# Performance work log

Hardware: AMD Instinct MI355X
Metric: run time of the kernel (lower is better)

The kernel has to match this reference:

```python
import jax, jax.numpy as jnp
import numpy as np

MARGIN = 0.3
EPS = 1e-12


def setup_inputs() -> dict:
    key = jax.random.key(0)
    k1, k2 = jax.random.split(key)
    inputs = jax.random.normal(k1, (256, 2048), dtype=jnp.float32)
    targets = jax.random.randint(k2, (256,), 0, 32, dtype=jnp.int64)
    return {"inputs": inputs, "targets": targets}


def reference(inputs, targets):
    # Pairwise Euclidean distance matrix [n, n] via GEMM.
    sq = jnp.sum(inputs * inputs, axis=1)                      # [n]
    dist = sq[:, None] + sq[None, :] - 2.0 * (inputs @ inputs.T)
    dist = jnp.sqrt(jnp.clip(dist, EPS, None))                 # [n, n]

    same = targets[:, None] == targets[None, :]                # [n, n]
    # Triplet margin for all (anchor, positive, negative) in one broadcast.
    tri = dist[:, :, None] - dist[:, None, :] + MARGIN         # [n, n, n]
    tri = jnp.clip(tri, EPS, None)
    # Valid: same label for (a, p), different label for (a, neg).
    valid = same[:, :, None] & (~same)[:, None, :]             # [n, n, n]
    # Torch version stacks only valid triplets (dynamic shape); here we
    # return the dense [n, n, n] tensor with invalid entries zeroed.
    return jnp.where(valid, tri, 0.0)
```

## Files before the change

### kernel.cpp

```cpp
#include <hip/hip_runtime.h>
#include <hip/hip_fp16.h>

#define N 256
#define D 2048
#define MARGIN_F 0.3f
#define EPS_F 1e-12f
#define SQRT_EPS_F 1e-6f
#define KSLICES 8

typedef float v4f __attribute__((ext_vector_type(4)));
typedef short bf16x8 __attribute__((ext_vector_type(8)));

static __device__ __forceinline__ unsigned short f2bf_rne(float f) {
    union { float f; unsigned u; } v; v.f = f;
    unsigned r = v.u + 0x7fffu + ((v.u >> 16) & 1u);
    return (unsigned short)(r >> 16);
}

__global__ __launch_bounds__(256) void conv_sq_kernel(const float* __restrict__ x,
                                                      unsigned short* __restrict__ xb,
                                                      float* __restrict__ sq) {
    __shared__ float red[4];
    const int row = blockIdx.x;
    const int tid = threadIdx.x;
    const float* xr = x + (size_t)row * D + tid * 8;
    float4 v0 = *(const float4*)(xr);
    float4 v1 = *(const float4*)(xr + 4);
    float acc = v0.x * v0.x + v0.y * v0.y + v0.z * v0.z + v0.w * v0.w +
                v1.x * v1.x + v1.y * v1.y + v1.z * v1.z + v1.w * v1.w;
    union { unsigned short h[8]; uint4 u; } pk;
    pk.h[0] = f2bf_rne(v0.x); pk.h[1] = f2bf_rne(v0.y);
    pk.h[2] = f2bf_rne(v0.z); pk.h[3] = f2bf_rne(v0.w);
    pk.h[4] = f2bf_rne(v1.x); pk.h[5] = f2bf_rne(v1.y);
    pk.h[6] = f2bf_rne(v1.z); pk.h[7] = f2bf_rne(v1.w);
    *(uint4*)(xb + (size_t)row * D + tid * 8) = pk.u;
#pragma unroll
    for (int off = 32; off > 0; off >>= 1) acc += __shfl_down(acc, off, 64);
    if ((tid & 63) == 0) red[tid >> 6] = acc;
    __syncthreads();
    if (tid == 0) sq[row] = red[0] + red[1] + red[2] + red[3];
}

__global__ __launch_bounds__(256) void gram_mfma_kernel(const unsigned short* __restrict__ xb,
                                                        float* __restrict__ part) {
    const int w = threadIdx.x >> 6;
    const int l = threadIdx.x & 63;
    const int i0 = blockIdx.x * 32 + (w >> 1) * 16;
    const int j0 = blockIdx.y * 32 + (w & 1) * 16;
    const int ks = blockIdx.z;
    const int kq = (l >> 4) * 8;
    const unsigned short* pa = xb + (size_t)(i0 + (l & 15)) * D + ks * 256 + kq;
    const unsigned short* pb = xb + (size_t)(j0 + (l & 15)) * D + ks * 256 + kq;
    v4f acc = {0.f, 0.f, 0.f, 0.f};
#pragma unroll
    for (int t = 0; t < 8; ++t) {
        bf16x8 af = *(const bf16x8*)(pa + t * 32);
        bf16x8 bf = *(const bf16x8*)(pb + t * 32);
        acc = __builtin_amdgcn_mfma_f32_16x16x32_bf16(af, bf, acc, 0, 0, 0);
    }
    float* pp = part + ((size_t)(i0 + (l >> 4) * 4) * KSLICES + ks) * N + j0 + (l & 15);
#pragma unroll
    for (int r = 0; r < 4; ++r)
        pp[(size_t)r * KSLICES * N] = acc[r];
}

__global__ __launch_bounds__(256) void fused_kernel(const float* __restrict__ part,
                                                    const float* __restrict__ sq,
                                                    const int* __restrict__ targets,
                                                    float* __restrict__ out) {
    __shared__ __align__(16) float drow[N];
    __shared__ int lab[N];
    const int a = blockIdx.x;
    const int tid = threadIdx.x;
    lab[tid] = targets[tid];

    const float* pr = part + (size_t)a * (KSLICES * N);
    float dot = 0.f;
#pragma unroll
    for (int ks = 0; ks < KSLICES; ++ks)
        dot += pr[ks * N + tid];
    drow[tid] = (tid == a) ? SQRT_EPS_F
                           : sqrtf(fmaxf(sq[a] + sq[tid] - 2.f * dot, EPS_F));
    __syncthreads();

    const int la = lab[a];
    const int lane = tid & 63;
    const int pq = tid >> 6;
    const int p0 = blockIdx.y * 64 + pq * 16;

    v4f dan = *(const v4f*)(drow + lane * 4);
    v4f mb = MARGIN_F - dan;
    v4f nokv = {(lab[lane * 4 + 0] != la) ? 1.f : 0.f,
                (lab[lane * 4 + 1] != la) ? 1.f : 0.f,
                (lab[lane * 4 + 2] != la) ? 1.f : 0.f,
                (lab[lane * 4 + 3] != la) ? 1.f : 0.f};

    float* obase = out + ((size_t)a << 16) + lane * 4;
#pragma unroll 4
    for (int i = 0; i < 16; ++i) {
        int p = p0 + i;
        v4f r = {0.f, 0.f, 0.f, 0.f};
        if (lab[p] == la) {
            float dap = drow[p];
            v4f t = dap + mb;
            t.x = fmaxf(t.x, EPS_F);
            t.y = fmaxf(t.y, EPS_F);
            t.z = fmaxf(t.z, EPS_F);
            t.w = fmaxf(t.w, EPS_F);
            r = t * nokv;
        }
        *(v4f*)(obase + (size_t)p * N) = r;
    }
}

__global__ __launch_bounds__(64) void sq_kernel(const float* __restrict__ x,
                                                float* __restrict__ sq) {
    int row = blockIdx.x;
    int lane = threadIdx.x;
    const float4* xr = (const float4*)(x + (size_t)row * D);
    float acc = 0.f;
#pragma unroll
    for (int it = 0; it < 8; ++it) {
        float4 v = xr[lane + 64 * it];
        acc += v.x * v.x + v.y * v.y + v.z * v.z + v.w * v.w;
    }
#pragma unroll
    for (int off = 32; off > 0; off >>= 1) acc += __shfl_down(acc, off, 64);
    if (lane == 0) sq[row] = acc;
}

__global__ __launch_bounds__(256) void gram_valu_kernel(const float* __restrict__ x,
                                                        __half* __restrict__ part) {
    __shared__ __align__(16) float As[64 * 68];
    __shared__ __align__(16) float Bs[64 * 68];
    const int i0 = blockIdx.x * 64, j0 = blockIdx.y * 64, k0 = blockIdx.z * 64;
    const int tid = threadIdx.x;
#pragma unroll
    for (int it = 0; it < 4; ++it) {
        int f = tid + 256 * it;
        int row = f >> 4;
        int c4 = f & 15;
        int sc4 = c4 ^ ((row >> 2) & 15);
        float4 va = *(const float4*)(x + (size_t)(i0 + row) * D + k0 + c4 * 4);
        float4 vb = *(const float4*)(x + (size_t)(j0 + row) * D + k0 + c4 * 4);
        *(float4*)(As + row * 68 + sc4 * 4) = va;
        *(float4*)(Bs + row * 68 + sc4 * 4) = vb;
    }
    __syncthreads();
    const int tx = tid & 15, ty = tid >> 4;
    float acc[4][4];
#pragma unroll
    for (int r = 0; r < 4; ++r)
#pragma unroll
        for (int c = 0; c < 4; ++c) acc[r][c] = 0.f;
#pragma unroll
    for (int k4 = 0; k4 < 16; ++k4) {
        float4 a[4], b[4];
        const int ca = (k4 ^ ty) << 2, cb = (k4 ^ tx) << 2;
#pragma unroll
        for (int r = 0; r < 4; ++r) {
            a[r] = *(const float4*)(As + (ty * 4 + r) * 68 + ca);
            b[r] = *(const float4*)(Bs + (tx * 4 + r) * 68 + cb);
        }
#pragma unroll
        for (int r = 0; r < 4; ++r)
#pragma unroll
            for (int c = 0; c < 4; ++c)
                acc[r][c] += a[r].x * b[c].x + a[r].y * b[c].y +
                             a[r].z * b[c].z + a[r].w * b[c].w;
    }
    __half* pout = part + (size_t)blockIdx.z * (N * N);
#pragma unroll
    for (int r = 0; r < 4; ++r) {
        int gi = i0 + ty * 4 + r;
        union { __half2 h2[2]; uint2 u; } pk;
        pk.h2[0] = __floats2half2_rn(acc[r][0], acc[r][1]);
        pk.h2[1] = __floats2half2_rn(acc[r][2], acc[r][3]);
        *(uint2*)(pout + (size_t)gi * N + j0 + tx * 4) = pk.u;
    }
}

__global__ __launch_bounds__(256) void dist_kernel(const __half* __restrict__ part,
                                                   const float* __restrict__ sq,
                                                   float* __restrict__ dist) {
    const int a = blockIdx.x;
    const int tid = threadIdx.x;
    float dot = 0.f;
    const __half* base = part + a * N + tid;
#pragma unroll 8
    for (int ks = 0; ks < 32; ++ks)
        dot += __half2float(base[(size_t)ks * (N * N)]);
    dist[a * N + tid] = (tid == a) ? SQRT_EPS_F
                                   : sqrtf(fmaxf(sq[a] + sq[tid] - 2.f * dot, EPS_F));
}

__global__ __launch_bounds__(256) void triplet_kernel(const float* __restrict__ dist,
                                                      const int* __restrict__ targets,
                                                      float* __restrict__ out) {
    __shared__ __align__(16) float drow[N];
    __shared__ int lab[N];
    const int a = blockIdx.x;
    const int p0 = blockIdx.y * 16;
    const int tid = threadIdx.x;
    lab[tid] = targets[tid];
    drow[tid] = dist[a * N + tid];
    __syncthreads();
    const int la = lab[a];
    const int lane = tid & 63;
    const int pq = tid >> 6;
    v4f dan = *(const v4f*)(drow + lane * 4);
    v4f mb = MARGIN_F - dan;
    v4f nokv = {(lab[lane * 4 + 0] != la) ? 1.f : 0.f,
                (lab[lane * 4 + 1] != la) ? 1.f : 0.f,
                (lab[lane * 4 + 2] != la) ? 1.f : 0.f,
                (lab[lane * 4 + 3] != la) ? 1.f : 0.f};
    float* obase = out + ((size_t)a << 16) + lane * 4;
#pragma unroll
    for (int j = 0; j < 4; ++j) {
        int p = p0 + pq * 4 + j;
        v4f r = {0.f, 0.f, 0.f, 0.f};
        if (lab[p] == la) {
            float dap = drow[p];
            v4f t = dap + mb;
            t.x = fmaxf(t.x, EPS_F);
            t.y = fmaxf(t.y, EPS_F);
            t.z = fmaxf(t.z, EPS_F);
            t.w = fmaxf(t.w, EPS_F);
            r = t * nokv;
        }
        *(v4f*)(obase + (size_t)p * N) = r;
    }
}

extern "C" void kernel_launch(void* const* d_in, const int* in_sizes, int n_in,
                              void* d_out, int out_size, void* d_ws, size_t ws_size,
                              hipStream_t stream) {
    const float* x = (const float*)d_in[0];
    const int* targets = (const int*)d_in[1];
    float* out = (float*)d_out;
    float* ws = (float*)d_ws;

    float* sq = ws;
    unsigned short* xb = (unsigned short*)(ws + 256);
    float* part = (float*)(xb + (size_t)N * D);
    size_t need = 256 * 4 + (size_t)N * D * 2 + (size_t)KSLICES * N * N * 4 + 1024;

    if (ws_size >= need) {
        conv_sq_kernel<<<256, 256, 0, stream>>>(x, xb, sq);
        gram_mfma_kernel<<<dim3(8, 8, KSLICES), 256, 0, stream>>>(xb, part);
        fused_kernel<<<dim3(256, 4), 256, 0, stream>>>(part, sq, targets, out);
    } else {
        __half* hpart = (__half*)d_out;
        float* sq2 = ws;
        float* dist = ws + 256;
        sq_kernel<<<256, 64, 0, stream>>>(x, sq2);
        gram_valu_kernel<<<dim3(4, 4, 32), 256, 0, stream>>>(x, hpart);
        dist_kernel<<<256, 256, 0, stream>>>(hpart, sq2, dist);
        triplet_kernel<<<dim3(256, 16), 256, 0, stream>>>(dist, targets, out);
    }
}
```

Before: 85.06 us.

## Fuse three kernels into one cooperative kernel with grid-wide syncs

Replaces the three launches (bf16 conversion with row norms, MFMA Gram, triplet output) with one cooperative kernel of 1024 blocks that uses grid.sync() between phases. This removes two kernel launch gaps. The split-K factor is doubled to 16 so the Gram phase fills all 1024 blocks, which doubles the partial-sum buffer and the reads of it in the final phase. Grid syncs add their own overhead, and the launch fails if 1024 blocks cannot all be resident at once.

```diff
diff --git a/kernel.cpp b/kernel.cpp
--- a/kernel.cpp
+++ b/kernel.cpp
@@ -1,12 +1,15 @@
 #include <hip/hip_runtime.h>
 #include <hip/hip_fp16.h>
+#include <hip/hip_cooperative_groups.h>
+
+namespace cg = cooperative_groups;
 
 #define N 256
 #define D 2048
 #define MARGIN_F 0.3f
 #define EPS_F 1e-12f
 #define SQRT_EPS_F 1e-6f
-#define KSLICES 8
+#define KSLICES 16
 
 typedef float v4f __attribute__((ext_vector_type(4)));
 typedef short bf16x8 __attribute__((ext_vector_type(8)));
@@ -17,99 +20,104 @@
     return (unsigned short)(r >> 16);
 }
 
-__global__ __launch_bounds__(256) void conv_sq_kernel(const float* __restrict__ x,
+__global__ __launch_bounds__(256, 4) void mega_kernel(const float* __restrict__ x,
+                                                      const int* __restrict__ targets,
                                                       unsigned short* __restrict__ xb,
-                                                      float* __restrict__ sq) {
-    __shared__ float red[4];
-    const int row = blockIdx.x;
-    const int tid = threadIdx.x;
-    const float* xr = x + (size_t)row * D + tid * 8;
-    float4 v0 = *(const float4*)(xr);
-    float4 v1 = *(const float4*)(xr + 4);
-    float acc = v0.x * v0.x + v0.y * v0.y + v0.z * v0.z + v0.w * v0.w +
-                v1.x * v1.x + v1.y * v1.y + v1.z * v1.z + v1.w * v1.w;
-    union { unsigned short h[8]; uint4 u; } pk;
-    pk.h[0] = f2bf_rne(v0.x); pk.h[1] = f2bf_rne(v0.y);
-    pk.h[2] = f2bf_rne(v0.z); pk.h[3] = f2bf_rne(v0.w);
-    pk.h[4] = f2bf_rne(v1.x); pk.h[5] = f2bf_rne(v1.y);
-    pk.h[6] = f2bf_rne(v1.z); pk.h[7] = f2bf_rne(v1.w);
-    *(uint4*)(xb + (size_t)row * D + tid * 8) = pk.u;
-#pragma unroll
-    for (int off = 32; off > 0; off >>= 1) acc += __shfl_down(acc, off, 64);
-    if ((tid & 63) == 0) red[tid >> 6] = acc;
-    __syncthreads();
-    if (tid == 0) sq[row] = red[0] + red[1] + red[2] + red[3];
-}
-
-__global__ __launch_bounds__(256) void gram_mfma_kernel(const unsigned short* __restrict__ xb,
-                                                        float* __restrict__ part) {
-    const int w = threadIdx.x >> 6;
-    const int l = threadIdx.x & 63;
-    const int i0 = blockIdx.x * 32 + (w >> 1) * 16;
-    const int j0 = blockIdx.y * 32 + (w & 1) * 16;
-    const int ks = blockIdx.z;
-    const int kq = (l >> 4) * 8;
-    const unsigned short* pa = xb + (size_t)(i0 + (l & 15)) * D + ks * 256 + kq;
-    const unsigned short* pb = xb + (size_t)(j0 + (l & 15)) * D + ks * 256 + kq;
-    v4f acc = {0.f, 0.f, 0.f, 0.f};
-#pragma unroll
-    for (int t = 0; t < 8; ++t) {
-        bf16x8 af = *(const bf16x8*)(pa + t * 32);
-        bf16x8 bf = *(const bf16x8*)(pb + t * 32);
-        acc = __builtin_amdgcn_mfma_f32_16x16x32_bf16(af, bf, acc, 0, 0, 0);
-    }
-    float* pp = part + ((size_t)(i0 + (l >> 4) * 4) * KSLICES + ks) * N + j0 + (l & 15);
-#pragma unroll
-    for (int r = 0; r < 4; ++r)
-        pp[(size_t)r * KSLICES * N] = acc[r];
-}
-
-__global__ __launch_bounds__(256) void fused_kernel(const float* __restrict__ part,
-                                                    const float* __restrict__ sq,
-                                                    const int* __restrict__ targets,
-                                                    float* __restrict__ out) {
+                                                      float* __restrict__ sq,
+                                                      float* __restrict__ part,
+                                                      float* __restrict__ out) {
+    cg::grid_group grid = cg::this_grid();
     __shared__ __align__(16) float drow[N];
     __shared__ int lab[N];
-    const int a = blockIdx.x;
-    const int tid = threadIdx.x;
-    lab[tid] = targets[tid];
-
-    const float* pr = part + (size_t)a * (KSLICES * N);
-    float dot = 0.f;
-#pragma unroll
-    for (int ks = 0; ks < KSLICES; ++ks)
-        dot += pr[ks * N + tid];
-    drow[tid] = (tid == a) ? SQRT_EPS_F
-                           : sqrtf(fmaxf(sq[a] + sq[tid] - 2.f * dot, EPS_F));
-    __syncthreads();
-
-    const int la = lab[a];
-    const int lane = tid & 63;
-    const int pq = tid >> 6;
-    const int p0 = blockIdx.y * 64 + pq * 16;
-
-    v4f dan = *(const v4f*)(drow + lane * 4);
-    v4f mb = MARGIN_F - dan;
-    v4f nokv = {(lab[lane * 4 + 0] != la) ? 1.f : 0.f,
-                (lab[lane * 4 + 1] != la) ? 1.f : 0.f,
-                (lab[lane * 4 + 2] != la) ? 1.f : 0.f,
-                (lab[lane * 4 + 3] != la) ? 1.f : 0.f};
-
-    float* obase = out + ((size_t)a << 16) + lane * 4;
+    __shared__ float red[4];
+    const int b = blockIdx.x;
+    const int tid = threadIdx.x;
+
+    if (b < 256) {
+        const float* xr = x + (size_t)b * D + tid * 8;
+        float4 v0 = *(const float4*)(xr);
+        float4 v1 = *(const float4*)(xr + 4);
+        float acc = v0.x * v0.x + v0.y * v0.y + v0.z * v0.z + v0.w * v0.w +
+                    v1.x * v1.x + v1.y * v1.y + v1.z * v1.z + v1.w * v1.w;
+        union { unsigned short h[8]; uint4 u; } pk;
+        pk.h[0] = f2bf_rne(v0.x); pk.h[1] = f2bf_rne(v0.y);
+        pk.h[2] = f2bf_rne(v0.z); pk.h[3] = f2bf_rne(v0.w);
+        pk.h[4] = f2bf_rne(v1.x); pk.h[5] = f2bf_rne(v1.y);
+        pk.h[6] = f2bf_rne(v1.z); pk.h[7] = f2bf_rne(v1.w);
+        *(uint4*)(xb + (size_t)b * D + tid * 8) = pk.u;
+#pragma unroll
+        for (int off = 32; off > 0; off >>= 1) acc += __shfl_down(acc, off, 64);
+        if ((tid & 63) == 0) red[tid >> 6] = acc;
+        __syncthreads();
+        if (tid == 0) sq[b] = red[0] + red[1] + red[2] + red[3];
+    }
+    grid.sync();
+
+    {
+        const int w = tid >> 6;
+        const int l = tid & 63;
+        const int i0 = (b & 7) * 32 + (w >> 1) * 16;
+        const int j0 = ((b >> 3) & 7) * 32 + (w & 1) * 16;
+        const int ks = b >> 6;
+        const int kq = (l >> 4) * 8;
+        const unsigned short* pa = xb + (size_t)(i0 + (l & 15)) * D + ks * 128 + kq;
+        const unsigned short* pb = xb + (size_t)(j0 + (l & 15)) * D + ks * 128 + kq;
+        v4f acc = {0.f, 0.f, 0.f, 0.f};
+#pragma unroll
+        for (int t = 0; t < 4; ++t) {
+            bf16x8 af = *(const bf16x8*)(pa + t * 32);
+            bf16x8 bf = *(const bf16x8*)(pb + t * 32);
+            acc = __builtin_amdgcn_mfma_f32_16x16x32_bf16(af, bf, acc, 0, 0, 0);
+        }
+        float* pp = part + ((size_t)(i0 + (l >> 4) * 4) * KSLICES + ks) * N + j0 + (l & 15);
+#pragma unroll
+        for (int r = 0; r < 4; ++r)
+            pp[(size_t)r * KSLICES * N] = acc[r];
+    }
+    grid.sync();
+
+    {
+        const int a = b & 255;
+        const int qy = b >> 8;
+        lab[tid] = targets[tid];
+
+        const float* pr = part + (size_t)a * (KSLICES * N);
+        float dot = 0.f;
+#pragma unroll
+        for (int ks = 0; ks < KSLICES; ++ks)
+            dot += pr[ks * N + tid];
+        drow[tid] = (tid == a) ? SQRT_EPS_F
+                               : sqrtf(fmaxf(sq[a] + sq[tid] - 2.f * dot, EPS_F));
+        __syncthreads();
+
+        const int la = lab[a];
+        const int lane = tid & 63;
+        const int pq = tid >> 6;
+        const int p0 = qy * 64 + pq * 16;
+
+        v4f dan = *(const v4f*)(drow + lane * 4);
+        v4f mb = MARGIN_F - dan;
+        v4f nokv = {(lab[lane * 4 + 0] != la) ? 1.f : 0.f,
+                    (lab[lane * 4 + 1] != la) ? 1.f : 0.f,
+                    (lab[lane * 4 + 2] != la) ? 1.f : 0.f,
+                    (lab[lane * 4 + 3] != la) ? 1.f : 0.f};
+
+        float* obase = out + ((size_t)a << 16) + lane * 4;
 #pragma unroll 4
-    for (int i = 0; i < 16; ++i) {
-        int p = p0 + i;
-        v4f r = {0.f, 0.f, 0.f, 0.f};
-        if (lab[p] == la) {
-            float dap = drow[p];
-            v4f t = dap + mb;
-            t.x = fmaxf(t.x, EPS_F);
-            t.y = fmaxf(t.y, EPS_F);
-            t.z = fmaxf(t.z, EPS_F);
-            t.w = fmaxf(t.w, EPS_F);
-            r = t * nokv;
-        }
-        *(v4f*)(obase + (size_t)p * N) = r;
+        for (int i = 0; i < 16; ++i) {
+            int p = p0 + i;
+            v4f r = {0.f, 0.f, 0.f, 0.f};
+            if (lab[p] == la) {
+                float dap = drow[p];
+                v4f t = dap + mb;
+                t.x = fmaxf(t.x, EPS_F);
+                t.y = fmaxf(t.y, EPS_F);
+                t.z = fmaxf(t.z, EPS_F);
+                t.w = fmaxf(t.w, EPS_F);
+                r = t * nokv;
+            }
+            *(v4f*)(obase + (size_t)p * N) = r;
+        }
     }
 }
 
@@ -246,9 +254,10 @@
     size_t need = 256 * 4 + (size_t)N * D * 2 + (size_t)KSLICES * N * N * 4 + 1024;
 
     if (ws_size >= need) {
-        conv_sq_kernel<<<256, 256, 0, stream>>>(x, xb, sq);
-        gram_mfma_kernel<<<dim3(8, 8, KSLICES), 256, 0, stream>>>(xb, part);
-        fused_kernel<<<dim3(256, 4), 256, 0, stream>>>(part, sq, targets, out);
+        void* args[] = {(void*)&x, (void*)&targets, (void*)&xb,
+                        (void*)&sq, (void*)&part, (void*)&out};
+        hipLaunchCooperativeKernel((const void*)mega_kernel, dim3(1024), dim3(256),
+                                   args, 0, stream);
     } else {
         __half* hpart = (__half*)d_out;
         float* sq2 = ws;
```

Result: slower. 320.7 us (+277.0%).
